# Kernel optimization log

Measured on AMD Instinct MI355X. Metric: run time of the kernel, lower is better.

Reference implementation:

```python
import jax, jax.numpy as jnp
import numpy as np

N, DIM_EMB, HIDDEN, OUT = 8192, 256, 128, 64


def setup_inputs() -> dict:
    key = jax.random.key(0)
    k1, k2, k3, k4 = jax.random.split(key, 4)
    x = jax.random.normal(k1, (N, DIM_EMB), dtype=jnp.float32)
    adj = jax.random.uniform(k2, (N, N), dtype=jnp.float32)
    # GraphConvolution params (Glorot-style init)
    s1 = 1.0 / np.sqrt(DIM_EMB)
    s2 = 1.0 / np.sqrt(HIDDEN)
    W1 = jax.random.uniform(k3, (DIM_EMB, HIDDEN), dtype=jnp.float32, minval=-s1, maxval=s1)
    b1 = jnp.zeros((HIDDEN,), dtype=jnp.float32)
    W2 = jax.random.uniform(k4, (HIDDEN, OUT), dtype=jnp.float32, minval=-s2, maxval=s2)
    b2 = jnp.zeros((OUT,), dtype=jnp.float32)
    return {"x": x, "adj": adj, "W1": W1, "b1": b1, "W2": W2, "b2": b2}


def _adj_hat(adj):
    # torch: adj.mm(diag(d)).t().mm(diag(d)) == diag(d) @ adj.T @ diag(d)
    # expressed as broadcast row/col scaling (no NxN diag matmuls)
    d = jnp.power(jnp.sum(adj, axis=1), -0.5)  # [N]
    return (adj * d[None, :]).T * d[None, :]


def reference(x, adj, W1, b1, W2, b2):
    A = _adj_hat(adj)                     # [N, N]
    h = A @ (x @ W1) + b1                 # GraphConvolution 1
    h = jax.nn.relu(h)                    # dropout is identity in eval
    out = A @ (h @ W2) + b2               # GraphConvolution 2
    return out
```

## Files before the change

kernel.cpp:

```cpp
#include <hip/hip_runtime.h>
#include <math.h>

typedef unsigned short u16;
typedef __attribute__((ext_vector_type(8))) short short8v;
typedef __attribute__((ext_vector_type(4))) float f32x4v;
typedef __attribute__((ext_vector_type(4))) unsigned short u16x4;

#define GLOAD_LDS16(src, dst)                                      \
  __builtin_amdgcn_global_load_lds(                                \
      (const __attribute__((address_space(1))) void*)(src),        \
      (__attribute__((address_space(3))) void*)(dst), 16, 0, 0)

__device__ __forceinline__ u16 f2bf(float f) {
  union { float f; unsigned u; } v; v.f = f;
  unsigned r = v.u + 0x7FFFu + ((v.u >> 16) & 1u);
  return (u16)(r >> 16);
}

__global__ __launch_bounds__(256) void k_adj(const float* __restrict__ adj,
                                             u16* __restrict__ adjT,
                                             float* __restrict__ rsP,
                                             const float4* __restrict__ x,
                                             u16x4* __restrict__ xbf,
                                             const float* __restrict__ W1,
                                             const float* __restrict__ W2,
                                             u16* __restrict__ W1T,
                                             u16* __restrict__ W2T) {
  __shared__ __align__(16) char Tsm[32768];
  const int tid = threadIdx.x, l = tid & 63, w = tid >> 6;
  const int bx = blockIdx.x, by = blockIdx.y;
  const int c0 = bx * 256, r0 = by * 64;
  const int flat = by * 32 + bx;

  if (tid < 128) {
    const int gid = flat * 128 + tid;
    const float4 v = x[gid];
    u16x4 o; o.x = f2bf(v.x); o.y = f2bf(v.y); o.z = f2bf(v.z); o.w = f2bf(v.w);
    xbf[gid] = o;
  }
  if (flat < 128) { const int gid = flat * 256 + tid; const int n = gid >> 8, c = gid & 255; W1T[gid] = f2bf(W1[c * 128 + n]); }
  if (flat < 32)  { const int gid = flat * 256 + tid; const int n = gid >> 7, c = gid & 127; W2T[gid] = f2bf(W2[c * 64 + n]); }

  const int g = l >> 4;
  const size_t rowbase = (size_t)(r0 + w * 4) * 8192 + c0 + l * 4;
#pragma unroll
  for (int p = 0; p < 4; ++p) {
    const float4 r0v = *(const float4*)(adj + rowbase + (size_t)(p * 16 + 0) * 8192);
    const float4 r1v = *(const float4*)(adj + rowbase + (size_t)(p * 16 + 1) * 8192);
    const float4 r2v = *(const float4*)(adj + rowbase + (size_t)(p * 16 + 2) * 8192);
    const float4 r3v = *(const float4*)(adj + rowbase + (size_t)(p * 16 + 3) * 8192);
    const int rrb = p * 16 + w * 4;
    {
      float s = r0v.x + r0v.y + r0v.z + r0v.w;
      s += __shfl_xor(s, 8, 64); s += __shfl_xor(s, 4, 64);
      s += __shfl_xor(s, 2, 64); s += __shfl_xor(s, 1, 64);
      if ((l & 15) == 0) rsP[(size_t)(bx * 4 + g) * 8192 + r0 + rrb + 0] = s;
    }
    {
      float s = r1v.x + r1v.y + r1v.z + r1v.w;
      s += __shfl_xor(s, 8, 64); s += __shfl_xor(s, 4, 64);
      s += __shfl_xor(s, 2, 64); s += __shfl_xor(s, 1, 64);
      if ((l & 15) == 0) rsP[(size_t)(bx * 4 + g) * 8192 + r0 + rrb + 1] = s;
    }
    {
      float s = r2v.x + r2v.y + r2v.z + r2v.w;
      s += __shfl_xor(s, 8, 64); s += __shfl_xor(s, 4, 64);
      s += __shfl_xor(s, 2, 64); s += __shfl_xor(s, 1, 64);
      if ((l & 15) == 0) rsP[(size_t)(bx * 4 + g) * 8192 + r0 + rrb + 2] = s;
    }
    {
      float s = r3v.x + r3v.y + r3v.z + r3v.w;
      s += __shfl_xor(s, 8, 64); s += __shfl_xor(s, 4, 64);
      s += __shfl_xor(s, 2, 64); s += __shfl_xor(s, 1, 64);
      if ((l & 15) == 0) rsP[(size_t)(bx * 4 + g) * 8192 + r0 + rrb + 3] = s;
    }
    const int slot = (p * 4 + w) ^ (l & 15);
    {
      u16x4 pk; pk.x = f2bf(r0v.x); pk.y = f2bf(r1v.x); pk.z = f2bf(r2v.x); pk.w = f2bf(r3v.x);
      *(u16x4*)(Tsm + (l * 4 + 0) * 128 + slot * 8) = pk;
    }
    {
      u16x4 pk; pk.x = f2bf(r0v.y); pk.y = f2bf(r1v.y); pk.z = f2bf(r2v.y); pk.w = f2bf(r3v.y);
      *(u16x4*)(Tsm + (l * 4 + 1) * 128 + slot * 8) = pk;
    }
    {
      u16x4 pk; pk.x = f2bf(r0v.z); pk.y = f2bf(r1v.z); pk.z = f2bf(r2v.z); pk.w = f2bf(r3v.z);
      *(u16x4*)(Tsm + (l * 4 + 2) * 128 + slot * 8) = pk;
    }
    {
      u16x4 pk; pk.x = f2bf(r0v.w); pk.y = f2bf(r1v.w); pk.z = f2bf(r2v.w); pk.w = f2bf(r3v.w);
      *(u16x4*)(Tsm + (l * 4 + 3) * 128 + slot * 8) = pk;
    }
  }
  __syncthreads();
#pragma unroll
  for (int it = 0; it < 8; ++it) {
    const int chunk = it * 256 + tid;
    const int c = chunk >> 3, part = chunk & 7;
    const int m = (c >> 2) & 15;
    const int s0 = (part * 2) ^ m, s1 = (part * 2 + 1) ^ m;
    const float2 lo = *(const float2*)(Tsm + c * 128 + s0 * 8);
    const float2 hi = *(const float2*)(Tsm + c * 128 + s1 * 8);
    float4 o; o.x = lo.x; o.y = lo.y; o.z = hi.x; o.w = hi.y;
    *(float4*)((char*)adjT + ((size_t)(c0 + c) * 8192 + r0 + part * 8) * 2) = o;
  }
}

__global__ __launch_bounds__(256) void k_d(const float* __restrict__ rsP,
                                           float* __restrict__ dv) {
  const int i = blockIdx.x * 256 + threadIdx.x;
  float s = 0.f;
#pragma unroll 8
  for (int cx = 0; cx < 128; ++cx) s += rsP[(size_t)cx * 8192 + i];
  dv[i] = 1.0f / sqrtf(s);
}

template <int BM, int BN, int EPI>
__global__ __launch_bounds__(256, 2) void gemm_kern(
    const u16* __restrict__ A, const u16* __restrict__ B,
    const float* __restrict__ dvec, float* __restrict__ Cp, u16* __restrict__ Ut,
    const int lda, const int ldb, const int ksteps) {
  constexpr int MREP = BM / 32;
  constexpr int NREP = BN / 32;
  __shared__ __align__(16) u16 smem[2 * BM * 64 + 2 * BN * 64];
  const int tid = threadIdx.x, l = tid & 63, w = tid >> 6;
  const int wm = w >> 1, wn = w & 1;
  const int m0 = blockIdx.x * BM;
  const int kbase = blockIdx.y * ksteps * 64;
  const u16* Ag = A + (size_t)m0 * lda + kbase;
  const u16* Bg = B + kbase;
  u16* Asm = smem;
  u16* Bsm = smem + 2 * BM * 64;

  f32x4v acc[MREP][NREP];
  const f32x4v zero = {0.f, 0.f, 0.f, 0.f};
#pragma unroll
  for (int mr = 0; mr < MREP; ++mr)
#pragma unroll
    for (int nr = 0; nr < NREP; ++nr) acc[mr][nr] = zero;

  auto stageA = [&](int k0, int buf) {
#pragma unroll
    for (int q = 0; q < BM / 32; ++q) {
      const int c = q * 256 + tid;
      const int row = c >> 3;
      const int kp = (c & 7) ^ (row & 7);
      const u16* src = Ag + (size_t)row * lda + k0 + kp * 8;
      u16* dst = Asm + buf * (BM * 64) + (q * 256 + (tid & ~63)) * 8;
      GLOAD_LDS16(src, dst);
    }
  };
  auto stageB = [&](int k0, int buf) {
#pragma unroll
    for (int q = 0; q < BN / 32; ++q) {
      const int c = q * 256 + tid;
      const int row = c >> 3;
      const int kp = (c & 7) ^ (row & 7);
      const u16* src = Bg + (size_t)row * ldb + k0 + kp * 8;
      u16* dst = Bsm + buf * (BN * 64) + (q * 256 + (tid & ~63)) * 8;
      GLOAD_LDS16(src, dst);
    }
  };

  stageA(0, 0);
  stageB(0, 0);

  for (int t = 0; t < ksteps; ++t) {
    const int cur = t & 1;
    __syncthreads();
    if (t + 1 < ksteps) { stageA((t + 1) * 64, cur ^ 1); stageB((t + 1) * 64, cur ^ 1); }
    const char* Ab = (const char*)(Asm + cur * (BM * 64));
    const char* Bb = (const char*)(Bsm + cur * (BN * 64));
#pragma unroll
    for (int kk = 0; kk < 2; ++kk) {
      short8v a[MREP], b[NREP];
#pragma unroll
      for (int mr = 0; mr < MREP; ++mr) {
        const int row = wm * (BM / 2) + mr * 16 + (l & 15);
        const int kb = kk * 64 + ((l >> 4) << 4);
        a[mr] = *(const short8v*)(Ab + row * 128 + (kb ^ ((row & 7) << 4)));
      }
#pragma unroll
      for (int nr = 0; nr < NREP; ++nr) {
        const int row = wn * (BN / 2) + nr * 16 + (l & 15);
        const int kb = kk * 64 + ((l >> 4) << 4);
        b[nr] = *(const short8v*)(Bb + row * 128 + (kb ^ ((row & 7) << 4)));
      }
#pragma unroll
      for (int mr = 0; mr < MREP; ++mr)
#pragma unroll
        for (int nr = 0; nr < NREP; ++nr)
          acc[mr][nr] = __builtin_amdgcn_mfma_f32_16x16x32_bf16(a[mr], b[nr],
                                                                acc[mr][nr], 0, 0, 0);
    }
  }

  if (EPI == 0) {
    float* outp = Cp + (size_t)blockIdx.y * ((size_t)8192 * BN);
#pragma unroll
    for (int mr = 0; mr < MREP; ++mr)
#pragma unroll
      for (int r = 0; r < 4; ++r) {
        const int m = m0 + wm * (BM / 2) + mr * 16 + ((l >> 4) << 2) + r;
#pragma unroll
        for (int nr = 0; nr < NREP; ++nr) {
          const int n = wn * (BN / 2) + nr * 16 + (l & 15);
          outp[(size_t)m * BN + n] = acc[mr][nr][r];
        }
      }
  } else {
    __syncthreads();
    u16* T = smem;
#pragma unroll
    for (int mr = 0; mr < MREP; ++mr)
#pragma unroll
      for (int r = 0; r < 4; ++r) {
        const int mloc = wm * (BM / 2) + mr * 16 + ((l >> 4) << 2) + r;
        const float dd = dvec[m0 + mloc];
#pragma unroll
        for (int nr = 0; nr < NREP; ++nr) {
          const int n = wn * (BN / 2) + nr * 16 + (l & 15);
          T[n * (BM + 8) + mloc] = f2bf(acc[mr][nr][r] * dd);
        }
      }
    __syncthreads();
#pragma unroll
    for (int it = 0; it < (BN * (BM / 8)) / 256; ++it) {
      const int chunk = it * 256 + tid;
      const int n = chunk / (BM / 8), part = chunk & (BM / 8 - 1);
      const float4 v = *(const float4*)(T + n * (BM + 8) + part * 8);
      *(float4*)((char*)Ut + ((size_t)n * 8192 + m0 + part * 8) * 2) = v;
    }
  }
}

__global__ __launch_bounds__(256) void k_e1(const float4* __restrict__ P,
                                            const float* __restrict__ dv,
                                            const float* __restrict__ b1,
                                            u16x4* __restrict__ h) {
  const int gid = blockIdx.x * 256 + threadIdx.x;
  const int STR = 262144;
  const float4 s0 = P[gid], s1 = P[gid + STR], s2 = P[gid + 2 * STR], s3 = P[gid + 3 * STR];
  const float dd = dv[gid >> 5];
  const float4 bb = ((const float4*)b1)[gid & 31];
  u16x4 o;
  o.x = f2bf(fmaxf(fmaf(dd, s0.x + s1.x + s2.x + s3.x, bb.x), 0.f));
  o.y = f2bf(fmaxf(fmaf(dd, s0.y + s1.y + s2.y + s3.y, bb.y), 0.f));
  o.z = f2bf(fmaxf(fmaf(dd, s0.z + s1.z + s2.z + s3.z, bb.z), 0.f));
  o.w = f2bf(fmaxf(fmaf(dd, s0.w + s1.w + s2.w + s3.w, bb.w), 0.f));
  h[gid] = o;
}

__global__ __launch_bounds__(256) void k_e2(const float4* __restrict__ P,
                                            const float* __restrict__ dv,
                                            const float* __restrict__ b2,
                                            float4* __restrict__ out) {
  const int gid = blockIdx.x * 256 + threadIdx.x;
  const int STR = 131072;
  const float4 s0 = P[gid], s1 = P[gid + STR], s2 = P[gid + 2 * STR], s3 = P[gid + 3 * STR];
  const float dd = dv[gid >> 4];
  const float4 bb = ((const float4*)b2)[gid & 15];
  float4 r;
  r.x = fmaf(dd, s0.x + s1.x + s2.x + s3.x, bb.x);
  r.y = fmaf(dd, s0.y + s1.y + s2.y + s3.y, bb.y);
  r.z = fmaf(dd, s0.z + s1.z + s2.z + s3.z, bb.z);
  r.w = fmaf(dd, s0.w + s1.w + s2.w + s3.w, bb.w);
  out[gid] = r;
}

extern "C" void kernel_launch(void* const* d_in, const int* in_sizes, int n_in,
                              void* d_out, int out_size, void* d_ws, size_t ws_size,
                              hipStream_t stream) {
  (void)in_sizes; (void)n_in; (void)out_size; (void)ws_size;
  const float* x   = (const float*)d_in[0];
  const float* adj = (const float*)d_in[1];
  const float* W1  = (const float*)d_in[2];
  const float* b1  = (const float*)d_in[3];
  const float* W2  = (const float*)d_in[4];
  const float* b2  = (const float*)d_in[5];
  float* out = (float*)d_out;
  char* ws = (char*)d_ws;

  u16*   adjT = (u16*)(ws + 0ull);
  float* T1p  = (float*)(ws + 134217728ull);
  float* T2p  = (float*)(ws + 151005184ull);
  u16*   xbf  = (u16*)(ws + 159393792ull);
  u16*   hbf  = (u16*)(ws + 163588096ull);
  u16*   U1T  = (u16*)(ws + 165685248ull);
  u16*   U2T  = (u16*)(ws + 167782400ull);
  u16*   W1T  = (u16*)(ws + 168830976ull);
  u16*   W2T  = (u16*)(ws + 168896512ull);
  float* dv   = (float*)(ws + 168912896ull);
  float* rsP  = T1p;

  k_adj<<<dim3(32, 128), 256, 0, stream>>>(adj, adjT, rsP,
                                           (const float4*)x, (u16x4*)xbf,
                                           W1, W2, W1T, W2T);
  k_d<<<32, 256, 0, stream>>>(rsP, dv);
  gemm_kern<64, 128, 1><<<dim3(128, 1), 256, 0, stream>>>(
      xbf, W1T, dv, nullptr, U1T, 256, 256, 4);
  gemm_kern<64, 128, 0><<<dim3(128, 4), 256, 0, stream>>>(
      adjT, U1T, nullptr, T1p, nullptr, 8192, 8192, 32);
  k_e1<<<1024, 256, 0, stream>>>((const float4*)T1p, dv, b1, (u16x4*)hbf);
  gemm_kern<64, 64, 1><<<dim3(128, 1), 256, 0, stream>>>(
      hbf, W2T, dv, nullptr, U2T, 128, 128, 2);
  gemm_kern<64, 64, 0><<<dim3(128, 4), 256, 0, stream>>>(
      adjT, U2T, nullptr, T2p, nullptr, 8192, 8192, 32);
  k_e2<<<512, 256, 0, stream>>>((const float4*)T2p, dv, b2, (float4*)out);
}
```

Measured before the change: 180.9 us.

## Fuse degree normalization into first GEMM and epilogue1 into h@W2 GEMM

```diff
diff --git a/kernel.cpp b/kernel.cpp
--- a/kernel.cpp
+++ b/kernel.cpp
@@ -106,23 +106,17 @@
   }
 }
 
-__global__ __launch_bounds__(256) void k_d(const float* __restrict__ rsP,
-                                           float* __restrict__ dv) {
-  const int i = blockIdx.x * 256 + threadIdx.x;
-  float s = 0.f;
-#pragma unroll 8
-  for (int cx = 0; cx < 128; ++cx) s += rsP[(size_t)cx * 8192 + i];
-  dv[i] = 1.0f / sqrtf(s);
-}
-
-template <int BM, int BN, int EPI>
+template <int BM, int BN, int EPI, int DSRC>
 __global__ __launch_bounds__(256, 2) void gemm_kern(
     const u16* __restrict__ A, const u16* __restrict__ B,
-    const float* __restrict__ dvec, float* __restrict__ Cp, u16* __restrict__ Ut,
+    const float* __restrict__ dvec, const float* __restrict__ rsP,
+    float* __restrict__ dvout, float* __restrict__ Cp, u16* __restrict__ Ut,
     const int lda, const int ldb, const int ksteps) {
   constexpr int MREP = BM / 32;
   constexpr int NREP = BN / 32;
   __shared__ __align__(16) u16 smem[2 * BM * 64 + 2 * BN * 64];
+  __shared__ float psum[(DSRC == 2) ? 4 : 1][64];
+  __shared__ float dv_sm[(DSRC == 2) ? 64 : 1];
   const int tid = threadIdx.x, l = tid & 63, w = tid >> 6;
   const int wm = w >> 1, wn = w & 1;
   const int m0 = blockIdx.x * BM;
@@ -132,6 +126,21 @@
   u16* Asm = smem;
   u16* Bsm = smem + 2 * BM * 64;
 
+  if (DSRC == 2) {
+    float s = 0.f;
+    const float* rp = rsP + (size_t)(w * 32) * 8192 + m0 + l;
+#pragma unroll 8
+    for (int q = 0; q < 32; ++q) s += rp[(size_t)q * 8192];
+    psum[w][l] = s;
+    __syncthreads();
+    if (tid < 64) {
+      const float dd = 1.0f / sqrtf(psum[0][tid] + psum[1][tid] + psum[2][tid] + psum[3][tid]);
+      dv_sm[tid] = dd;
+      dvout[m0 + tid] = dd;
+    }
+    __syncthreads();
+  }
+
   f32x4v acc[MREP][NREP];
   const f32x4v zero = {0.f, 0.f, 0.f, 0.f};
 #pragma unroll
@@ -216,7 +225,7 @@
 #pragma unroll
       for (int r = 0; r < 4; ++r) {
         const int mloc = wm * (BM / 2) + mr * 16 + ((l >> 4) << 2) + r;
-        const float dd = dvec[m0 + mloc];
+        const float dd = (DSRC == 2) ? dv_sm[mloc] : dvec[m0 + mloc];
 #pragma unroll
         for (int nr = 0; nr < NREP; ++nr) {
           const int n = wn * (BN / 2) + nr * 16 + (l & 15);
@@ -234,21 +243,111 @@
   }
 }
 
-__global__ __launch_bounds__(256) void k_e1(const float4* __restrict__ P,
-                                            const float* __restrict__ dv,
-                                            const float* __restrict__ b1,
-                                            u16x4* __restrict__ h) {
-  const int gid = blockIdx.x * 256 + threadIdx.x;
-  const int STR = 262144;
-  const float4 s0 = P[gid], s1 = P[gid + STR], s2 = P[gid + 2 * STR], s3 = P[gid + 3 * STR];
-  const float dd = dv[gid >> 5];
-  const float4 bb = ((const float4*)b1)[gid & 31];
-  u16x4 o;
-  o.x = f2bf(fmaxf(fmaf(dd, s0.x + s1.x + s2.x + s3.x, bb.x), 0.f));
-  o.y = f2bf(fmaxf(fmaf(dd, s0.y + s1.y + s2.y + s3.y, bb.y), 0.f));
-  o.z = f2bf(fmaxf(fmaf(dd, s0.z + s1.z + s2.z + s3.z, bb.z), 0.f));
-  o.w = f2bf(fmaxf(fmaf(dd, s0.w + s1.w + s2.w + s3.w, bb.w), 0.f));
-  h[gid] = o;
+__global__ __launch_bounds__(256, 2) void k_g3(const float* __restrict__ T1p,
+                                               const u16* __restrict__ W2T,
+                                               const float* __restrict__ dv,
+                                               const float* __restrict__ b1,
+                                               u16* __restrict__ U2T) {
+  __shared__ __align__(16) u16 smem[2 * 4096 + 2 * 4096];
+  const int tid = threadIdx.x, l = tid & 63, w = tid >> 6;
+  const int wm = w >> 1, wn = w & 1;
+  const int m0 = blockIdx.x * 64;
+  u16* Asm = smem;
+  u16* Bsm = smem + 8192;
+
+#pragma unroll
+  for (int buf = 0; buf < 2; ++buf)
+#pragma unroll
+    for (int q = 0; q < 2; ++q) {
+      const int c = q * 256 + tid;
+      const int row = c >> 3;
+      const int kp = (c & 7) ^ (row & 7);
+      const u16* src = W2T + row * 128 + buf * 64 + kp * 8;
+      u16* dst = Bsm + buf * 4096 + (q * 256 + (tid & ~63)) * 8;
+      GLOAD_LDS16(src, dst);
+    }
+
+  const float* P0 = T1p + (size_t)m0 * 128;
+#pragma unroll
+  for (int it = 0; it < 8; ++it) {
+    const int f = it * 256 + tid;
+    const int row = f >> 5, n4 = f & 31;
+    const float* p = P0 + (size_t)row * 128 + n4 * 4;
+    const float4 s0 = *(const float4*)(p);
+    const float4 s1 = *(const float4*)(p + (size_t)1048576);
+    const float4 s2 = *(const float4*)(p + (size_t)2097152);
+    const float4 s3 = *(const float4*)(p + (size_t)3145728);
+    const float dd = dv[m0 + row];
+    const float4 bb = ((const float4*)b1)[n4];
+    u16x4 pk;
+    pk.x = f2bf(fmaxf(fmaf(dd, s0.x + s1.x + s2.x + s3.x, bb.x), 0.f));
+    pk.y = f2bf(fmaxf(fmaf(dd, s0.y + s1.y + s2.y + s3.y, bb.y), 0.f));
+    pk.z = f2bf(fmaxf(fmaf(dd, s0.z + s1.z + s2.z + s3.z, bb.z), 0.f));
+    pk.w = f2bf(fmaxf(fmaf(dd, s0.w + s1.w + s2.w + s3.w, bb.w), 0.f));
+    const int kc_g = n4 >> 1;
+    const int buf = kc_g >> 3, kc = kc_g & 7;
+    const int slot = kc ^ (row & 7);
+    *(u16x4*)((char*)Asm + buf * 8192 + row * 128 + slot * 16 + (n4 & 1) * 8) = pk;
+  }
+  __syncthreads();
+
+  f32x4v acc[2][2];
+  const f32x4v zero = {0.f, 0.f, 0.f, 0.f};
+#pragma unroll
+  for (int mr = 0; mr < 2; ++mr)
+#pragma unroll
+    for (int nr = 0; nr < 2; ++nr) acc[mr][nr] = zero;
+
+#pragma unroll
+  for (int t = 0; t < 2; ++t) {
+    const char* Ab = (const char*)(Asm + t * 4096);
+    const char* Bb = (const char*)(Bsm + t * 4096);
+#pragma unroll
+    for (int kk = 0; kk < 2; ++kk) {
+      short8v a[2], b[2];
+#pragma unroll
+      for (int mr = 0; mr < 2; ++mr) {
+        const int row = wm * 32 + mr * 16 + (l & 15);
+        const int kb = kk * 64 + ((l >> 4) << 4);
+        a[mr] = *(const short8v*)(Ab + row * 128 + (kb ^ ((row & 7) << 4)));
+      }
+#pragma unroll
+      for (int nr = 0; nr < 2; ++nr) {
+        const int row = wn * 32 + nr * 16 + (l & 15);
+        const int kb = kk * 64 + ((l >> 4) << 4);
+        b[nr] = *(const short8v*)(Bb + row * 128 + (kb ^ ((row & 7) << 4)));
+      }
+#pragma unroll
+      for (int mr = 0; mr < 2; ++mr)
+#pragma unroll
+        for (int nr = 0; nr < 2; ++nr)
+          acc[mr][nr] = __builtin_amdgcn_mfma_f32_16x16x32_bf16(a[mr], b[nr],
+                                                                acc[mr][nr], 0, 0, 0);
+    }
+  }
+
+  __syncthreads();
+  u16* T = smem;
+#pragma unroll
+  for (int mr = 0; mr < 2; ++mr)
+#pragma unroll
+    for (int r = 0; r < 4; ++r) {
+      const int mloc = wm * 32 + mr * 16 + ((l >> 4) << 2) + r;
+      const float dd = dv[m0 + mloc];
+#pragma unroll
+      for (int nr = 0; nr < 2; ++nr) {
+        const int n = wn * 32 + nr * 16 + (l & 15);
+        T[n * 72 + mloc] = f2bf(acc[mr][nr][r] * dd);
+      }
+    }
+  __syncthreads();
+#pragma unroll
+  for (int it = 0; it < 2; ++it) {
+    const int chunk = it * 256 + tid;
+    const int n = chunk >> 3, part = chunk & 7;
+    const float4 v = *(const float4*)(T + n * 72 + part * 8);
+    *(float4*)((char*)U2T + ((size_t)n * 8192 + m0 + part * 8) * 2) = v;
+  }
 }
 
 __global__ __launch_bounds__(256) void k_e2(const float4* __restrict__ P,
@@ -285,7 +384,6 @@
   float* T1p  = (float*)(ws + 134217728ull);
   float* T2p  = (float*)(ws + 151005184ull);
   u16*   xbf  = (u16*)(ws + 159393792ull);
-  u16*   hbf  = (u16*)(ws + 163588096ull);
   u16*   U1T  = (u16*)(ws + 165685248ull);
   u16*   U2T  = (u16*)(ws + 167782400ull);
   u16*   W1T  = (u16*)(ws + 168830976ull);
@@ -296,15 +394,12 @@
   k_adj<<<dim3(32, 128), 256, 0, stream>>>(adj, adjT, rsP,
                                            (const float4*)x, (u16x4*)xbf,
                                            W1, W2, W1T, W2T);
-  k_d<<<32, 256, 0, stream>>>(rsP, dv);
-  gemm_kern<64, 128, 1><<<dim3(128, 1), 256, 0, stream>>>(
-      xbf, W1T, dv, nullptr, U1T, 256, 256, 4);
-  gemm_kern<64, 128, 0><<<dim3(128, 4), 256, 0, stream>>>(
-      adjT, U1T, nullptr, T1p, nullptr, 8192, 8192, 32);
-  k_e1<<<1024, 256, 0, stream>>>((const float4*)T1p, dv, b1, (u16x4*)hbf);
-  gemm_kern<64, 64, 1><<<dim3(128, 1), 256, 0, stream>>>(
-      hbf, W2T, dv, nullptr, U2T, 128, 128, 2);
-  gemm_kern<64, 64, 0><<<dim3(128, 4), 256, 0, stream>>>(
-      adjT, U2T, nullptr, T2p, nullptr, 8192, 8192, 32);
+  gemm_kern<64, 128, 1, 2><<<dim3(128, 1), 256, 0, stream>>>(
+      xbf, W1T, nullptr, rsP, dv, nullptr, U1T, 256, 256, 4);
+  gemm_kern<64, 128, 0, 0><<<dim3(128, 4), 256, 0, stream>>>(
+      adjT, U1T, nullptr, nullptr, nullptr, T1p, nullptr, 8192, 8192, 32);
+  k_g3<<<128, 256, 0, stream>>>(T1p, W2T, dv, b1, U2T);
+  gemm_kern<64, 64, 0, 0><<<dim3(128, 4), 256, 0, stream>>>(
+      adjT, U2T, nullptr, nullptr, nullptr, T2p, nullptr, 8192, 8192, 32);
   k_e2<<<512, 256, 0, stream>>>((const float4*)T2p, dv, b2, (float4*)out);
 }
```

New measurement: 171.6 us. 5.2% less time.
